# Kernel tuning notes

Hardware: AMD Instinct MI355X
Metric: run time of the kernel (lower is better)

Reference implementation:

```python
import jax, jax.numpy as jnp
import numpy as np

H1, W1GRID, K_SIZE, B = 28, 28, 5, 512
K2 = K_SIZE * K_SIZE  # 25 kernel weight matrices
_BITS = np.array([[0, 0], [0, 1], [1, 0], [1, 1]])  # 2^dim basis combos


def _grid_edges(h, w):
    """8-neighborhood grid graph; returns (src, dst, pseudo in [0,1]^2)."""
    ys, xs = np.meshgrid(np.arange(h), np.arange(w), indexing='ij')
    node = (ys * w + xs).reshape(-1)
    ys, xs = ys.reshape(-1), xs.reshape(-1)
    srcs, dsts, pses = [], [], []
    for dy in (-1, 0, 1):
        for dx in (-1, 0, 1):
            if dy == 0 and dx == 0:
                continue
            ny, nx = ys + dy, xs + dx
            ok = (ny >= 0) & (ny < h) & (nx >= 0) & (nx < w)
            srcs.append((ny * w + nx)[ok])   # neighbor j
            dsts.append(node[ok])            # center i
            p = np.array([[(dx + 1) / 2.0, (dy + 1) / 2.0]], dtype=np.float32)
            pses.append(np.repeat(p, ok.sum(), axis=0))
    return (np.concatenate(srcs), np.concatenate(dsts), np.concatenate(pses))


def _batched_graph(h, w, batch):
    s, d, p = _grid_edges(h, w)
    n = h * w
    off = (np.arange(batch, dtype=np.int64) * n)[:, None]
    src = (s[None, :] + off).reshape(-1)
    dst = (d[None, :] + off).reshape(-1)
    pse = np.tile(p, (batch, 1))
    return np.stack([src, dst]), pse


def setup_inputs() -> dict:
    key = jax.random.key(0)
    ks = jax.random.split(key, 8)
    e1, p1 = _batched_graph(28, 28, B)
    e2, p2 = _batched_graph(14, 14, B)
    return {
        'x': jax.random.uniform(ks[0], (B * 784, 1), jnp.float32),
        'pseudo1': jnp.asarray(p1), 'pseudo2': jnp.asarray(p2),
        'W1': jax.random.normal(ks[1], (K2, 1, 32), jnp.float32) * 0.2,
        'root1': jax.random.normal(ks[2], (1, 32), jnp.float32) * 0.2,
        'b1': jnp.zeros((32,), jnp.float32),
        'W2': jax.random.normal(ks[3], (K2, 32, 64), jnp.float32) * 0.05,
        'root2': jax.random.normal(ks[4], (32, 64), jnp.float32) * 0.05,
        'b2': jnp.zeros((64,), jnp.float32),
        'fc1_w': jax.random.normal(ks[5], (3136, 512), jnp.float32) * 0.02,
        'fc1_b': jnp.zeros((512,), jnp.float32),
        'fc2_w': jax.random.normal(ks[6], (512, 10), jnp.float32) * 0.05,
        'fc2_b': jnp.zeros((10,), jnp.float32),
        'edge_index1': jnp.asarray(e1, jnp.int64 if jax.config.jax_enable_x64 else jnp.int32),
        'edge_index2': jnp.asarray(e2, jnp.int64 if jax.config.jax_enable_x64 else jnp.int32),
    }


def _spline_basis(pseudo, k):
    # open B-spline, degree 1: each dim contributes 2 knots with linear weights
    frac = pseudo * (k - 1)                                   # [E,2]
    lo = jnp.clip(jnp.floor(frac), 0, k - 2)
    f = frac - lo                                             # [E,2]
    w = jnp.stack([1.0 - f, f], axis=-1)                      # [E,2,2]
    idx = jnp.stack([lo, lo + 1], axis=-1).astype(jnp.int32)  # [E,2,2]
    basis = w[:, 0, _BITS[:, 0]] * w[:, 1, _BITS[:, 1]]       # [E,4]
    widx = idx[:, 0, _BITS[:, 0]] + idx[:, 1, _BITS[:, 1]] * k  # [E,4]
    return basis, widx


def _spline_conv(x, edge_index, pseudo, W, root, bias, n_nodes, k):
    src, dst = edge_index[0], edge_index[1]
    x_j = x[src]                                              # [E,Cin] gather
    basis, widx = _spline_basis(pseudo, k)                    # [E,4]
    kk = k * k
    flat = (dst[:, None] * kk + widx).reshape(-1)             # [E*4]
    contrib = (basis[:, :, None] * x_j[:, None, :]).reshape(-1, x.shape[1])
    S = jnp.zeros((n_nodes * kk, x.shape[1]), x.dtype).at[flat].add(contrib)
    S = S.reshape(n_nodes, kk, x.shape[1])                    # per-node per-kernel sums
    deg = jnp.zeros((n_nodes,), x.dtype).at[dst].add(1.0)
    out = jnp.einsum('nki,kio->no', S, W) / jnp.maximum(deg, 1.0)[:, None]
    return out + x @ root + bias


def _pool2x2(x, b, hw, c):
    return x.reshape(b, hw // 2, 2, hw // 2, 2, c).max(axis=(2, 4))


def reference(x, pseudo1, pseudo2, W1, root1, b1, W2, root2, b2,
              fc1_w, fc1_b, fc2_w, fc2_b, edge_index1, edge_index2):
    n1 = x.shape[0]
    b = n1 // 784
    h = jax.nn.elu(_spline_conv(x, edge_index1, pseudo1, W1, root1, b1, n1, K_SIZE))
    h = _pool2x2(h, b, 28, 32).reshape(-1, 32)                # [B*196,32]
    h = jax.nn.elu(_spline_conv(h, edge_index2, pseudo2, W2, root2, b2, b * 196, K_SIZE))
    h = _pool2x2(h, b, 14, 64).reshape(-1, 7 * 7 * 64)        # [B,3136]
    h = jax.nn.elu(h @ fc1_w + fc1_b)
    # dropout is identity in eval mode
    h = jax.nn.elu(h @ fc2_w + fc2_b)
    return jax.nn.log_softmax(h, axis=-1)
```

## Files before the change

kernel.cpp:

```cpp
#include <hip/hip_runtime.h>
#include <math.h>

#define BATCH 512

__device__ __forceinline__ float elu1(float v) {
    return v > 0.f ? v : expm1f(v);
}

__global__ __launch_bounds__(256) void k1_conv1_pool(
    const float* __restrict__ x, const float* __restrict__ W1,
    const float* __restrict__ root1, const float* __restrict__ b1,
    float* __restrict__ p1) {
    __shared__ float xs[900];
    __shared__ float w1s[8 * 32 + 64];
    const int b = blockIdx.x;
    const int t = threadIdx.x;

    for (int l = t; l < 900; l += 256) xs[l] = 0.f;
    {
        int d = t >> 5, c = t & 31;
        int e = d + (d >= 4 ? 1 : 0);
        int dy = e / 3 - 1, dx = e % 3 - 1;
        int widx = 2 * (dx + 1) + 10 * (dy + 1);
        w1s[t] = W1[widx * 32 + c];
        if (t < 32) { w1s[256 + t] = root1[t]; w1s[288 + t] = b1[t]; }
    }
    __syncthreads();
    const float* xb = x + (size_t)b * 784;
    for (int l = t; l < 784; l += 256) {
        int y = l / 28, xx = l % 28;
        xs[(y + 1) * 30 + xx + 1] = xb[l];
    }
    __syncthreads();

    if (t >= 196) return;
    int py = t / 14, px = t % 14;
    int xbse[4];
    float xc[4], inv[4];
    #pragma unroll
    for (int p = 0; p < 4; ++p) {
        int sy = p >> 1, sx = p & 1;
        int y = 2 * py + sy, xx = 2 * px + sx;
        xbse[p] = (y + 1) * 30 + xx + 1;
        xc[p] = xs[xbse[p]];
        int nvy = 3 - (y == 0) - (y == 27);
        int nvx = 3 - (xx == 0) - (xx == 27);
        inv[p] = 1.f / (float)(nvy * nvx - 1);
    }
    const float4* w4 = (const float4*)w1s;
    float* outp = p1 + ((size_t)b * 196 + t) * 32;

    #pragma unroll
    for (int h = 0; h < 2; ++h) {
        float4 acc[4][4];
        #pragma unroll
        for (int p = 0; p < 4; ++p)
            #pragma unroll
            for (int q = 0; q < 4; ++q) acc[p][q] = make_float4(0.f, 0.f, 0.f, 0.f);
        #pragma unroll
        for (int d = 0; d < 8; ++d) {
            int e = d + (d >= 4 ? 1 : 0);
            int od = (e / 3 - 1) * 30 + (e % 3 - 1);
            float4 w0 = w4[d * 8 + h * 4 + 0];
            float4 w1 = w4[d * 8 + h * 4 + 1];
            float4 w2 = w4[d * 8 + h * 4 + 2];
            float4 w3 = w4[d * 8 + h * 4 + 3];
            #pragma unroll
            for (int p = 0; p < 4; ++p) {
                float xv = xs[xbse[p] + od];
                acc[p][0].x += xv * w0.x; acc[p][0].y += xv * w0.y; acc[p][0].z += xv * w0.z; acc[p][0].w += xv * w0.w;
                acc[p][1].x += xv * w1.x; acc[p][1].y += xv * w1.y; acc[p][1].z += xv * w1.z; acc[p][1].w += xv * w1.w;
                acc[p][2].x += xv * w2.x; acc[p][2].y += xv * w2.y; acc[p][2].z += xv * w2.z; acc[p][2].w += xv * w2.w;
                acc[p][3].x += xv * w3.x; acc[p][3].y += xv * w3.y; acc[p][3].z += xv * w3.z; acc[p][3].w += xv * w3.w;
            }
        }
        #pragma unroll
        for (int q = 0; q < 4; ++q) {
            float4 rt = w4[64 + h * 4 + q];
            float4 bs = w4[72 + h * 4 + q];
            float4 m = make_float4(-1e30f, -1e30f, -1e30f, -1e30f);
            #pragma unroll
            for (int p = 0; p < 4; ++p) {
                float4 v;
                v.x = elu1(acc[p][q].x * inv[p] + xc[p] * rt.x + bs.x);
                v.y = elu1(acc[p][q].y * inv[p] + xc[p] * rt.y + bs.y);
                v.z = elu1(acc[p][q].z * inv[p] + xc[p] * rt.z + bs.z);
                v.w = elu1(acc[p][q].w * inv[p] + xc[p] * rt.w + bs.w);
                m.x = fmaxf(m.x, v.x); m.y = fmaxf(m.y, v.y);
                m.z = fmaxf(m.z, v.z); m.w = fmaxf(m.w, v.w);
            }
            *(float4*)(outp + h * 16 + q * 4) = m;
        }
    }
}

__global__ __launch_bounds__(256) void k2_conv2_pool(
    const float* __restrict__ p1, const float* __restrict__ W2,
    const float* __restrict__ root2, const float* __restrict__ b2,
    float* __restrict__ p2) {
    __shared__ float xs[9216];
    __shared__ float wb[2304];
    const int b = blockIdx.x;
    const int t = threadIdx.x;
    int tile = t >> 3; if (tile > 27) tile = 27;
    const int cg = t & 7;

    static const int widx_t[8] = {0, 2, 4, 10, 14, 20, 22, 24};
    static const int ddy[8] = {-1,-1,-1, 0, 0, 1, 1, 1};
    static const int ddx[8] = {-1, 0, 1,-1, 1,-1, 0, 1};

    {
        const float4* s4 = (const float4*)W2;
        float4 v0 = s4[t], v1 = s4[t + 256];
        *(float4*)(wb + (t >> 4) * 72 + (t & 15) * 4) = v0;
        *(float4*)(wb + ((t + 256) >> 4) * 72 + (t & 15) * 4) = v1;
    }
    for (int l = t; l < 9216; l += 256) xs[l] = 0.f;
    __syncthreads();
    {
        const float* src = p1 + (size_t)b * 6272;
        for (int l = t; l < 6272; l += 256) {
            int node = l >> 5, i = l & 31;
            int y = node / 14, xx = node - y * 14;
            int np = (y + 1) * 16 + xx + 1;
            xs[np * 36 + 4 * ((i >> 2) ^ ((np >> 4) & 7)) + (i & 3)] = src[l];
        }
    }
    __syncthreads();

    const int py = tile >> 2, q = tile & 3;
    int npb[8]; float invd[8];
    #pragma unroll
    for (int p = 0; p < 8; ++p) {
        int r = p >> 2, c = p & 3;
        int gy = 2 * py + r, gx = 4 * q + c;
        npb[p] = (gy + 1) * 16 + gx + 1;
        int gxc = gx > 13 ? 13 : gx;
        int nvy = 3 - (gy == 0) - (gy == 13);
        int nvx = 3 - (gxc == 0) - (gxc == 13);
        invd[p] = 1.f / (float)(nvy * nvx - 1);
    }

    float4 acc[8][2];
    #pragma unroll
    for (int p = 0; p < 8; ++p) { acc[p][0] = make_float4(0,0,0,0); acc[p][1] = make_float4(0,0,0,0); }

    for (int d = 0; d < 9; ++d) {
        float4 pf0, pf1;
        if (d < 8) {
            const float* nsrc = (d + 1 == 8) ? root2 : (W2 + (size_t)widx_t[d + 1] * 2048);
            pf0 = ((const float4*)nsrc)[t];
            pf1 = ((const float4*)nsrc)[t + 256];
        }
        if (d == 8) {
            #pragma unroll
            for (int p = 0; p < 8; ++p) {
                acc[p][0].x *= invd[p]; acc[p][0].y *= invd[p]; acc[p][0].z *= invd[p]; acc[p][0].w *= invd[p];
                acc[p][1].x *= invd[p]; acc[p][1].y *= invd[p]; acc[p][1].z *= invd[p]; acc[p][1].w *= invd[p];
            }
        }
        int dnode = (d < 8) ? (ddy[d] * 16 + ddx[d]) : 0;
        int ax[8], sz[8];
        #pragma unroll
        for (int p = 0; p < 8; ++p) {
            int np = npb[p] + dnode;
            ax[p] = np * 36;
            sz[p] = (np >> 4) & 7;
        }
        #pragma unroll 2
        for (int i4 = 0; i4 < 8; ++i4) {
            float xa[8][4];
            #pragma unroll
            for (int p = 0; p < 8; ++p) {
                float4 v = *(const float4*)(xs + ax[p] + 4 * (i4 ^ sz[p]));
                xa[p][0] = v.x; xa[p][1] = v.y; xa[p][2] = v.z; xa[p][3] = v.w;
            }
            #pragma unroll
            for (int ii = 0; ii < 4; ++ii) {
                const float* wr = wb + (i4 * 4 + ii) * 72 + cg * 8;
                float4 w0 = *(const float4*)wr;
                float4 w1 = *(const float4*)(wr + 4);
                #pragma unroll
                for (int p = 0; p < 8; ++p) {
                    float xv = xa[p][ii];
                    acc[p][0].x += xv * w0.x; acc[p][0].y += xv * w0.y;
                    acc[p][0].z += xv * w0.z; acc[p][0].w += xv * w0.w;
                    acc[p][1].x += xv * w1.x; acc[p][1].y += xv * w1.y;
                    acc[p][1].z += xv * w1.z; acc[p][1].w += xv * w1.w;
                }
            }
        }
        if (d < 8) {
            __syncthreads();
            *(float4*)(wb + (t >> 4) * 72 + (t & 15) * 4) = pf0;
            *(float4*)(wb + ((t + 256) >> 4) * 72 + (t & 15) * 4) = pf1;
            __syncthreads();
        }
    }

    if (t < 224) {
        float4 bs0 = *(const float4*)(b2 + cg * 8);
        float4 bs1 = *(const float4*)(b2 + cg * 8 + 4);
        float* outb = p2 + (size_t)b * 3136;
        #pragma unroll
        for (int cc = 0; cc < 2; ++cc) {
            int cellcol = 2 * q + cc;
            if (cellcol > 6) continue;
            float4 m0 = make_float4(-1e30f,-1e30f,-1e30f,-1e30f);
            float4 m1 = m0;
            #pragma unroll
            for (int r = 0; r < 2; ++r)
            #pragma unroll
            for (int c2 = 0; c2 < 2; ++c2) {
                int p = r * 4 + cc * 2 + c2;
                float4 v0, v1;
                v0.x = elu1(acc[p][0].x + bs0.x); v0.y = elu1(acc[p][0].y + bs0.y);
                v0.z = elu1(acc[p][0].z + bs0.z); v0.w = elu1(acc[p][0].w + bs0.w);
                v1.x = elu1(acc[p][1].x + bs1.x); v1.y = elu1(acc[p][1].y + bs1.y);
                v1.z = elu1(acc[p][1].z + bs1.z); v1.w = elu1(acc[p][1].w + bs1.w);
                m0.x = fmaxf(m0.x, v0.x); m0.y = fmaxf(m0.y, v0.y);
                m0.z = fmaxf(m0.z, v0.z); m0.w = fmaxf(m0.w, v0.w);
                m1.x = fmaxf(m1.x, v1.x); m1.y = fmaxf(m1.y, v1.y);
                m1.z = fmaxf(m1.z, v1.z); m1.w = fmaxf(m1.w, v1.w);
            }
            int cell = py * 7 + cellcol;
            *(float4*)(outb + cell * 64 + cg * 8)     = m0;
            *(float4*)(outb + cell * 64 + cg * 8 + 4) = m1;
        }
    }
}

__global__ __launch_bounds__(256) void k3a_fc1(
    const float* __restrict__ A, const float* __restrict__ B,
    float* __restrict__ part) {
    __shared__ float As[2][16][64];
    __shared__ float Bs[2][16][72];
    const int t = threadIdx.x;
    const int tx = t & 15, ty = t >> 4;
    const int n0 = blockIdx.x * 64, m0 = blockIdx.y * 64;
    const int k0 = blockIdx.z * 272;
    const int steps = ((blockIdx.z == 11) ? 144 : 272) >> 4;

    const int sm = t & 63, k4 = t >> 6;
    const int sk = t >> 4, sc = t & 15;
    const float* Ap = A + (size_t)(m0 + sm) * 3136 + k0 + k4 * 4;
    const float* Bp = B + (size_t)(k0 + sk) * 512 + n0 + sc * 4;

    {
        float4 av = *(const float4*)Ap;
        float4 bv = *(const float4*)Bp;
        As[0][k4 * 4 + 0][sm] = av.x; As[0][k4 * 4 + 1][sm] = av.y;
        As[0][k4 * 4 + 2][sm] = av.z; As[0][k4 * 4 + 3][sm] = av.w;
        *(float4*)&Bs[0][sk][sc * 4] = bv;
    }
    __syncthreads();

    float acc[4][4];
    #pragma unroll
    for (int r = 0; r < 4; ++r)
        #pragma unroll
        for (int c = 0; c < 4; ++c) acc[r][c] = 0.f;

    for (int s = 0; s < steps; ++s) {
        float4 a0, b0;
        if (s + 1 < steps) {
            a0 = *(const float4*)(Ap + (s + 1) * 16);
            b0 = *(const float4*)(Bp + (size_t)(s + 1) * 16 * 512);
        }
        const int cur = s & 1;
        #pragma unroll
        for (int k = 0; k < 16; ++k) {
            float4 a4 = *(const float4*)&As[cur][k][ty * 4];
            float4 b4 = *(const float4*)&Bs[cur][k][tx * 4];
            acc[0][0] += a4.x * b4.x; acc[0][1] += a4.x * b4.y; acc[0][2] += a4.x * b4.z; acc[0][3] += a4.x * b4.w;
            acc[1][0] += a4.y * b4.x; acc[1][1] += a4.y * b4.y; acc[1][2] += a4.y * b4.z; acc[1][3] += a4.y * b4.w;
            acc[2][0] += a4.z * b4.x; acc[2][1] += a4.z * b4.y; acc[2][2] += a4.z * b4.z; acc[2][3] += a4.z * b4.w;
            acc[3][0] += a4.w * b4.x; acc[3][1] += a4.w * b4.y; acc[3][2] += a4.w * b4.z; acc[3][3] += a4.w * b4.w;
        }
        if (s + 1 < steps) {
            const int nxt = cur ^ 1;
            As[nxt][k4 * 4 + 0][sm] = a0.x; As[nxt][k4 * 4 + 1][sm] = a0.y;
            As[nxt][k4 * 4 + 2][sm] = a0.z; As[nxt][k4 * 4 + 3][sm] = a0.w;
            *(float4*)&Bs[nxt][sk][sc * 4] = b0;
        }
        __syncthreads();
    }

    float* pbase = part + ((size_t)blockIdx.z * 512 + m0 + ty * 4) * 512 + n0;
    #pragma unroll
    for (int r = 0; r < 4; ++r)
        *(float4*)(pbase + (size_t)r * 512 + tx * 4) =
            make_float4(acc[r][0], acc[r][1], acc[r][2], acc[r][3]);
}

__global__ __launch_bounds__(256) void k34_reduce_fc2_lsm(
    const float* __restrict__ part, const float* __restrict__ fc1b,
    const float* __restrict__ w, const float* __restrict__ fc2b,
    float* __restrict__ out, int KZ) {
    __shared__ float red[4][10];
    const int b = blockIdx.x, t = threadIdx.x;

    float a0 = fc1b[t], a1 = fc1b[t + 256];
    for (int kz = 0; kz < KZ; ++kz) {
        const float* pr = part + ((size_t)kz * 512 + b) * 512;
        a0 += pr[t]; a1 += pr[t + 256];
    }
    a0 = elu1(a0); a1 = elu1(a1);

    float acc[10];
    #pragma unroll
    for (int o = 0; o < 10; ++o)
        acc[o] = a0 * w[t * 10 + o] + a1 * w[(t + 256) * 10 + o];
    #pragma unroll
    for (int s = 32; s; s >>= 1)
        #pragma unroll
        for (int o = 0; o < 10; ++o) acc[o] += __shfl_xor(acc[o], s, 64);
    if ((t & 63) == 0) {
        #pragma unroll
        for (int o = 0; o < 10; ++o) red[t >> 6][o] = acc[o];
    }
    __syncthreads();
    if (t == 0) {
        float v[10], m = -1e30f;
        #pragma unroll
        for (int o = 0; o < 10; ++o) {
            float s = red[0][o] + red[1][o] + red[2][o] + red[3][o] + fc2b[o];
            v[o] = elu1(s);
            m = fmaxf(m, v[o]);
        }
        float ssum = 0.f;
        #pragma unroll
        for (int o = 0; o < 10; ++o) ssum += expf(v[o] - m);
        float lse = m + logf(ssum);
        #pragma unroll
        for (int o = 0; o < 10; ++o) out[(size_t)b * 10 + o] = v[o] - lse;
    }
}

extern "C" void kernel_launch(void* const* d_in, const int* in_sizes, int n_in,
                              void* d_out, int out_size, void* d_ws, size_t ws_size,
                              hipStream_t stream) {
    const float* x     = (const float*)d_in[0];
    const float* W1    = (const float*)d_in[3];
    const float* root1 = (const float*)d_in[4];
    const float* b1v   = (const float*)d_in[5];
    const float* W2    = (const float*)d_in[6];
    const float* root2 = (const float*)d_in[7];
    const float* b2v   = (const float*)d_in[8];
    const float* fc1w  = (const float*)d_in[9];
    const float* fc1b  = (const float*)d_in[10];
    const float* fc2w  = (const float*)d_in[11];
    const float* fc2b  = (const float*)d_in[12];

    float* ws = (float*)d_ws;
    float* p1 = ws;
    float* p2 = p1 + (size_t)BATCH * 196 * 32;
    float* part = p1;

    k1_conv1_pool<<<dim3(BATCH), 256, 0, stream>>>(x, W1, root1, b1v, p1);
    k2_conv2_pool<<<dim3(BATCH), 256, 0, stream>>>(p1, W2, root2, b2v, p2);
    k3a_fc1<<<dim3(8, 8, 12), 256, 0, stream>>>(p2, fc1w, part);
    k34_reduce_fc2_lsm<<<dim3(BATCH), 256, 0, stream>>>(part, fc1b, fc2w, fc2b, (float*)d_out, 12);
}
```

Baseline: 127.6 us.

## Fuse conv1+pool into conv2 kernel, keeping pooled features in shared memory

Merges the first spline conv + pool kernel into the second conv kernel, so each block writes its pooled 14x14x32 features straight into the swizzled padded shared-memory tile instead of round-tripping through global memory. Only the halo border of the conv2 input tile is zeroed now, rather than the whole tile. This removes one launch and the global write/read of the intermediate activation. In exchange the fused kernel uses more shared memory (about 50KB), which may lower occupancy, and conv1 runs on only 196 of the 256 threads.

After: 118.4 us. -7.2%, faster.

```diff
diff --git a/kernel.cpp b/kernel.cpp
--- a/kernel.cpp
+++ b/kernel.cpp
@@ -7,16 +7,23 @@
     return v > 0.f ? v : expm1f(v);
 }
 
-__global__ __launch_bounds__(256) void k1_conv1_pool(
+__global__ __launch_bounds__(256) void k12_conv12(
     const float* __restrict__ x, const float* __restrict__ W1,
     const float* __restrict__ root1, const float* __restrict__ b1,
-    float* __restrict__ p1) {
-    __shared__ float xs[900];
-    __shared__ float w1s[8 * 32 + 64];
+    const float* __restrict__ W2, const float* __restrict__ root2,
+    const float* __restrict__ b2, float* __restrict__ p2) {
+    __shared__ float xs1[900];
+    __shared__ float w1s[320];
+    __shared__ float xs2[9216];
+    __shared__ float wb[2304];
     const int b = blockIdx.x;
     const int t = threadIdx.x;
 
-    for (int l = t; l < 900; l += 256) xs[l] = 0.f;
+    static const int widx_t[8] = {0, 2, 4, 10, 14, 20, 22, 24};
+    static const int ddy[8] = {-1,-1,-1, 0, 0, 1, 1, 1};
+    static const int ddx[8] = {-1, 0, 1,-1, 1,-1, 0, 1};
+
+    for (int l = t; l < 900; l += 256) xs1[l] = 0.f;
     {
         int d = t >> 5, c = t & 31;
         int e = d + (d >= 4 ? 1 : 0);
@@ -25,115 +32,108 @@
         w1s[t] = W1[widx * 32 + c];
         if (t < 32) { w1s[256 + t] = root1[t]; w1s[288 + t] = b1[t]; }
     }
-    __syncthreads();
-    const float* xb = x + (size_t)b * 784;
-    for (int l = t; l < 784; l += 256) {
-        int y = l / 28, xx = l % 28;
-        xs[(y + 1) * 30 + xx + 1] = xb[l];
-    }
-    __syncthreads();
-
-    if (t >= 196) return;
-    int py = t / 14, px = t % 14;
-    int xbse[4];
-    float xc[4], inv[4];
-    #pragma unroll
-    for (int p = 0; p < 4; ++p) {
-        int sy = p >> 1, sx = p & 1;
-        int y = 2 * py + sy, xx = 2 * px + sx;
-        xbse[p] = (y + 1) * 30 + xx + 1;
-        xc[p] = xs[xbse[p]];
-        int nvy = 3 - (y == 0) - (y == 27);
-        int nvx = 3 - (xx == 0) - (xx == 27);
-        inv[p] = 1.f / (float)(nvy * nvx - 1);
-    }
-    const float4* w4 = (const float4*)w1s;
-    float* outp = p1 + ((size_t)b * 196 + t) * 32;
-
-    #pragma unroll
-    for (int h = 0; h < 2; ++h) {
-        float4 acc[4][4];
-        #pragma unroll
-        for (int p = 0; p < 4; ++p)
-            #pragma unroll
-            for (int q = 0; q < 4; ++q) acc[p][q] = make_float4(0.f, 0.f, 0.f, 0.f);
-        #pragma unroll
-        for (int d = 0; d < 8; ++d) {
-            int e = d + (d >= 4 ? 1 : 0);
-            int od = (e / 3 - 1) * 30 + (e % 3 - 1);
-            float4 w0 = w4[d * 8 + h * 4 + 0];
-            float4 w1 = w4[d * 8 + h * 4 + 1];
-            float4 w2 = w4[d * 8 + h * 4 + 2];
-            float4 w3 = w4[d * 8 + h * 4 + 3];
-            #pragma unroll
-            for (int p = 0; p < 4; ++p) {
-                float xv = xs[xbse[p] + od];
-                acc[p][0].x += xv * w0.x; acc[p][0].y += xv * w0.y; acc[p][0].z += xv * w0.z; acc[p][0].w += xv * w0.w;
-                acc[p][1].x += xv * w1.x; acc[p][1].y += xv * w1.y; acc[p][1].z += xv * w1.z; acc[p][1].w += xv * w1.w;
-                acc[p][2].x += xv * w2.x; acc[p][2].y += xv * w2.y; acc[p][2].z += xv * w2.z; acc[p][2].w += xv * w2.w;
-                acc[p][3].x += xv * w3.x; acc[p][3].y += xv * w3.y; acc[p][3].z += xv * w3.z; acc[p][3].w += xv * w3.w;
-            }
-        }
-        #pragma unroll
-        for (int q = 0; q < 4; ++q) {
-            float4 rt = w4[64 + h * 4 + q];
-            float4 bs = w4[72 + h * 4 + q];
-            float4 m = make_float4(-1e30f, -1e30f, -1e30f, -1e30f);
-            #pragma unroll
-            for (int p = 0; p < 4; ++p) {
-                float4 v;
-                v.x = elu1(acc[p][q].x * inv[p] + xc[p] * rt.x + bs.x);
-                v.y = elu1(acc[p][q].y * inv[p] + xc[p] * rt.y + bs.y);
-                v.z = elu1(acc[p][q].z * inv[p] + xc[p] * rt.z + bs.z);
-                v.w = elu1(acc[p][q].w * inv[p] + xc[p] * rt.w + bs.w);
-                m.x = fmaxf(m.x, v.x); m.y = fmaxf(m.y, v.y);
-                m.z = fmaxf(m.z, v.z); m.w = fmaxf(m.w, v.w);
-            }
-            *(float4*)(outp + h * 16 + q * 4) = m;
-        }
-    }
-}
-
-__global__ __launch_bounds__(256) void k2_conv2_pool(
-    const float* __restrict__ p1, const float* __restrict__ W2,
-    const float* __restrict__ root2, const float* __restrict__ b2,
-    float* __restrict__ p2) {
-    __shared__ float xs[9216];
-    __shared__ float wb[2304];
-    const int b = blockIdx.x;
-    const int t = threadIdx.x;
-    int tile = t >> 3; if (tile > 27) tile = 27;
-    const int cg = t & 7;
-
-    static const int widx_t[8] = {0, 2, 4, 10, 14, 20, 22, 24};
-    static const int ddy[8] = {-1,-1,-1, 0, 0, 1, 1, 1};
-    static const int ddx[8] = {-1, 0, 1,-1, 1,-1, 0, 1};
-
     {
         const float4* s4 = (const float4*)W2;
         float4 v0 = s4[t], v1 = s4[t + 256];
         *(float4*)(wb + (t >> 4) * 72 + (t & 15) * 4) = v0;
         *(float4*)(wb + ((t + 256) >> 4) * 72 + (t & 15) * 4) = v1;
     }
-    for (int l = t; l < 9216; l += 256) xs[l] = 0.f;
-    __syncthreads();
-    {
-        const float* src = p1 + (size_t)b * 6272;
-        for (int l = t; l < 6272; l += 256) {
-            int node = l >> 5, i = l & 31;
-            int y = node / 14, xx = node - y * 14;
-            int np = (y + 1) * 16 + xx + 1;
-            xs[np * 36 + 4 * ((i >> 2) ^ ((np >> 4) & 7)) + (i & 3)] = src[l];
-        }
-    }
-    __syncthreads();
-
-    const int py = tile >> 2, q = tile & 3;
+    {
+        float4 z = make_float4(0.f, 0.f, 0.f, 0.f);
+        float4* x4 = (float4*)xs2;
+        for (int l = t; l < 540; l += 256) {
+            int nd = l / 9, s = l - nd * 9;
+            int y, xx;
+            if (nd < 16)      { y = 0;       xx = nd; }
+            else if (nd < 32) { y = 15;      xx = nd - 16; }
+            else if (nd < 46) { y = nd - 31; xx = 0; }
+            else              { y = nd - 45; xx = 15; }
+            x4[(y * 16 + xx) * 9 + s] = z;
+        }
+    }
+    __syncthreads();
+    {
+        const float* xb = x + (size_t)b * 784;
+        for (int l = t; l < 784; l += 256) {
+            int y = l / 28, xx = l % 28;
+            xs1[(y + 1) * 30 + xx + 1] = xb[l];
+        }
+    }
+    __syncthreads();
+
+    if (t < 196) {
+        int py = t / 14, px = t % 14;
+        int xbse[4];
+        float xc[4], inv1[4];
+        #pragma unroll
+        for (int p = 0; p < 4; ++p) {
+            int sy = p >> 1, sx = p & 1;
+            int y = 2 * py + sy, xx = 2 * px + sx;
+            xbse[p] = (y + 1) * 30 + xx + 1;
+            xc[p] = xs1[xbse[p]];
+            int nvy = 3 - (y == 0) - (y == 27);
+            int nvx = 3 - (xx == 0) - (xx == 27);
+            inv1[p] = 1.f / (float)(nvy * nvx - 1);
+        }
+        const float4* w4 = (const float4*)w1s;
+        const int npw = (py + 1) * 16 + px + 1;
+        const int szw = (py + 1) & 7;
+        float* outp = xs2 + npw * 36;
+
+        #pragma unroll
+        for (int h = 0; h < 2; ++h) {
+            float4 acc[4][4];
+            #pragma unroll
+            for (int p = 0; p < 4; ++p)
+                #pragma unroll
+                for (int q = 0; q < 4; ++q) acc[p][q] = make_float4(0.f, 0.f, 0.f, 0.f);
+            #pragma unroll
+            for (int d = 0; d < 8; ++d) {
+                int e = d + (d >= 4 ? 1 : 0);
+                int od = (e / 3 - 1) * 30 + (e % 3 - 1);
+                float4 w0 = w4[d * 8 + h * 4 + 0];
+                float4 w1 = w4[d * 8 + h * 4 + 1];
+                float4 w2 = w4[d * 8 + h * 4 + 2];
+                float4 w3 = w4[d * 8 + h * 4 + 3];
+                #pragma unroll
+                for (int p = 0; p < 4; ++p) {
+                    float xv = xs1[xbse[p] + od];
+                    acc[p][0].x += xv * w0.x; acc[p][0].y += xv * w0.y; acc[p][0].z += xv * w0.z; acc[p][0].w += xv * w0.w;
+                    acc[p][1].x += xv * w1.x; acc[p][1].y += xv * w1.y; acc[p][1].z += xv * w1.z; acc[p][1].w += xv * w1.w;
+                    acc[p][2].x += xv * w2.x; acc[p][2].y += xv * w2.y; acc[p][2].z += xv * w2.z; acc[p][2].w += xv * w2.w;
+                    acc[p][3].x += xv * w3.x; acc[p][3].y += xv * w3.y; acc[p][3].z += xv * w3.z; acc[p][3].w += xv * w3.w;
+                }
+            }
+            #pragma unroll
+            for (int q = 0; q < 4; ++q) {
+                float4 rt = w4[64 + h * 4 + q];
+                float4 bs = w4[72 + h * 4 + q];
+                float4 m = make_float4(-1e30f, -1e30f, -1e30f, -1e30f);
+                #pragma unroll
+                for (int p = 0; p < 4; ++p) {
+                    float4 v;
+                    v.x = elu1(acc[p][q].x * inv1[p] + xc[p] * rt.x + bs.x);
+                    v.y = elu1(acc[p][q].y * inv1[p] + xc[p] * rt.y + bs.y);
+                    v.z = elu1(acc[p][q].z * inv1[p] + xc[p] * rt.z + bs.z);
+                    v.w = elu1(acc[p][q].w * inv1[p] + xc[p] * rt.w + bs.w);
+                    m.x = fmaxf(m.x, v.x); m.y = fmaxf(m.y, v.y);
+                    m.z = fmaxf(m.z, v.z); m.w = fmaxf(m.w, v.w);
+                }
+                int B = h * 4 + q;
+                *(float4*)(outp + 4 * (B ^ szw)) = m;
+            }
+        }
+    }
+    __syncthreads();
+
+    int tile = t >> 3; if (tile > 27) tile = 27;
+    const int cg = t & 7;
+    const int py2 = tile >> 2, q2 = tile & 3;
     int npb[8]; float invd[8];
     #pragma unroll
     for (int p = 0; p < 8; ++p) {
         int r = p >> 2, c = p & 3;
-        int gy = 2 * py + r, gx = 4 * q + c;
+        int gy = 2 * py2 + r, gx = 4 * q2 + c;
         npb[p] = (gy + 1) * 16 + gx + 1;
         int gxc = gx > 13 ? 13 : gx;
         int nvy = 3 - (gy == 0) - (gy == 13);
@@ -172,7 +172,7 @@
             float xa[8][4];
             #pragma unroll
             for (int p = 0; p < 8; ++p) {
-                float4 v = *(const float4*)(xs + ax[p] + 4 * (i4 ^ sz[p]));
+                float4 v = *(const float4*)(xs2 + ax[p] + 4 * (i4 ^ sz[p]));
                 xa[p][0] = v.x; xa[p][1] = v.y; xa[p][2] = v.z; xa[p][3] = v.w;
             }
             #pragma unroll
@@ -204,7 +204,7 @@
         float* outb = p2 + (size_t)b * 3136;
         #pragma unroll
         for (int cc = 0; cc < 2; ++cc) {
-            int cellcol = 2 * q + cc;
+            int cellcol = 2 * q2 + cc;
             if (cellcol > 6) continue;
             float4 m0 = make_float4(-1e30f,-1e30f,-1e30f,-1e30f);
             float4 m1 = m0;
@@ -223,7 +223,7 @@
                 m1.x = fmaxf(m1.x, v1.x); m1.y = fmaxf(m1.y, v1.y);
                 m1.z = fmaxf(m1.z, v1.z); m1.w = fmaxf(m1.w, v1.w);
             }
-            int cell = py * 7 + cellcol;
+            int cell = py2 * 7 + cellcol;
             *(float4*)(outb + cell * 64 + cg * 8)     = m0;
             *(float4*)(outb + cell * 64 + cg * 8 + 4) = m1;
         }
@@ -353,12 +353,10 @@
     const float* fc2b  = (const float*)d_in[12];
 
     float* ws = (float*)d_ws;
-    float* p1 = ws;
-    float* p2 = p1 + (size_t)BATCH * 196 * 32;
-    float* part = p1;
-
-    k1_conv1_pool<<<dim3(BATCH), 256, 0, stream>>>(x, W1, root1, b1v, p1);
-    k2_conv2_pool<<<dim3(BATCH), 256, 0, stream>>>(p1, W2, root2, b2v, p2);
+    float* part = ws;
+    float* p2 = ws + 3211264;
+
+    k12_conv12<<<dim3(BATCH), 256, 0, stream>>>(x, W1, root1, b1v, W2, root2, b2v, p2);
     k3a_fc1<<<dim3(8, 8, 12), 256, 0, stream>>>(p2, fc1w, part);
     k34_reduce_fc2_lsm<<<dim3(BATCH), 256, 0, stream>>>(part, fc1b, fc2w, fc2b, (float*)d_out, 12);
 }
```
